# Kernel optimization log

Measured on AMD Instinct MI355X. Metric: run time of the kernel, lower is better.

## Reference

```python
import jax, jax.numpy as jnp
import numpy as np

D = 1024
H = 16
T = D // H  # head dim; attention() scales by sqrt(Q.size(2)) == sqrt(T)
B = 4
S = 2048


def setup_inputs() -> dict:
    key = jax.random.key(0)
    ks = jax.random.split(key, 11)
    lim = 1.0 / np.sqrt(D)  # nn.Linear default init range
    inp = {
        "Q": jax.random.normal(ks[0], (B, S, D), jnp.float32),
        "K": jax.random.normal(ks[1], (B, S, D), jnp.float32),
        "V": jax.random.normal(ks[2], (B, S, D), jnp.float32),
        # per-head Q/K/V projections, stacked: weight [h, t, d], bias [h, t]
        "Wq": jax.random.uniform(ks[3], (H, T, D), jnp.float32, -lim, lim),
        "bq": jax.random.uniform(ks[4], (H, T), jnp.float32, -lim, lim),
        "Wk": jax.random.uniform(ks[5], (H, T, D), jnp.float32, -lim, lim),
        "bk": jax.random.uniform(ks[6], (H, T), jnp.float32, -lim, lim),
        "Wv": jax.random.uniform(ks[7], (H, T, D), jnp.float32, -lim, lim),
        "bv": jax.random.uniform(ks[8], (H, T), jnp.float32, -lim, lim),
        # output projection d -> d
        "Wo": jax.random.uniform(ks[9], (D, D), jnp.float32, -lim, lim),
        "bo": jax.random.uniform(ks[10], (D,), jnp.float32, -lim, lim),
    }
    return inp


def reference(Q, K, V, Wq, bq, Wk, bk, Wv, bv, Wo, bo):
    # Per-head projections, batched over heads: [b, h, s, t]
    q = jnp.einsum("bsd,htd->bhst", Q, Wq) + bq[None, :, None, :]
    k = jnp.einsum("bsd,htd->bhst", K, Wk) + bk[None, :, None, :]
    v = jnp.einsum("bsd,htd->bhst", V, Wv) + bv[None, :, None, :]
    # scaled dot-product attention; scale uses head dim T (Q.size(2) in source)
    scores = jnp.einsum("bhqt,bhkt->bhqk", q, k) / jnp.sqrt(jnp.asarray(T, q.dtype))
    probs = jax.nn.softmax(scores, axis=-1)
    ctx = jnp.einsum("bhqk,bhkt->bhqt", probs, v)
    # concat heads along feature dim (head i -> slice [i*t:(i+1)*t])
    z = ctx.transpose(0, 2, 1, 3).reshape(B, S, D)
    return jnp.einsum("bsd,ed->bse", z, Wo) + bo
```

## Files before the change

### kernel.cpp

```cpp
#include <hip/hip_runtime.h>

typedef unsigned short u16;
typedef unsigned int u32;
typedef __bf16 bf16x8 __attribute__((ext_vector_type(8)));
typedef __bf16 bf16x2 __attribute__((ext_vector_type(2)));
typedef float f32x4 __attribute__((ext_vector_type(4)));
typedef float f32x16 __attribute__((ext_vector_type(16)));
typedef unsigned int u32x2v __attribute__((ext_vector_type(2)));

#define BB 4
#define SS 2048
#define DD 1024
#define HH 16
#define TT 64

#define QSCALE 0.18033688011112042f

__device__ __forceinline__ u16 f32_to_bf16(float f) {
    unsigned int u = __float_as_uint(f);
    u += 0x7fffu + ((u >> 16) & 1u);
    return (u16)(u >> 16);
}

__device__ __forceinline__ u32 pack_bf16x2(float a, float b) {
    bf16x2 t;
    t[0] = (__bf16)a;
    t[1] = (__bf16)b;
    return __builtin_bit_cast(u32, t);
}

__device__ __forceinline__ void pswap(u32& x, u32& y) {
#if __has_builtin(__builtin_amdgcn_permlane32_swap)
    u32x2v r = __builtin_amdgcn_permlane32_swap(x, y, false, false);
    x = r[0];
    y = r[1];
#else
    u32 sx = __shfl_xor(y, 32);
    u32 sy = __shfl_xor(x, 32);
    bool lo = (threadIdx.x & 32) == 0;
    u32 nx = lo ? x : sx;
    u32 ny = lo ? sy : y;
    x = nx;
    y = ny;
#endif
}

#define GLDS(g, l) __builtin_amdgcn_global_load_lds(                              \
    (const __attribute__((address_space(1))) void*)(g),                            \
    (__attribute__((address_space(3))) void*)(l), 16, 0, 0)

struct PackArgs {
    const float* s[4];
    u16* d[4];
};

__global__ __launch_bounds__(256) void pack_multi(PackArgs a) {
    const float* __restrict__ src = a.s[blockIdx.y];
    u16* __restrict__ dst = a.d[blockIdx.y];
    int i = (blockIdx.x * 256 + threadIdx.x) * 8;
    float4 x = *(const float4*)(src + i);
    float4 y = *(const float4*)(src + i + 4);
    ushort4 o0, o1;
    o0.x = f32_to_bf16(x.x); o0.y = f32_to_bf16(x.y);
    o0.z = f32_to_bf16(x.z); o0.w = f32_to_bf16(x.w);
    o1.x = f32_to_bf16(y.x); o1.y = f32_to_bf16(y.y);
    o1.z = f32_to_bf16(y.z); o1.w = f32_to_bf16(y.w);
    *(ushort4*)(dst + i)     = o0;
    *(ushort4*)(dst + i + 4) = o1;
}

#define GEMM_CORE(Aptr, Wptr)                                                      \
    __shared__ u16 lds_a[128 * 64];                                                \
    __shared__ u16 lds_b[128 * 64];                                                \
    const int tid = threadIdx.x;                                                   \
    const int w = tid >> 6, l = tid & 63;                                          \
    const int bm = blockIdx.y * 128;                                               \
    const int bn = blockIdx.x * 128;                                               \
    const int wm = (w >> 1) * 64;                                                  \
    const int wn = (w & 1) * 64;                                                   \
    const int srow = l >> 3;                                                       \
    const int scol = (l & 7) * 16;                                                 \
    f32x4 acc[4][4] = {};                                                          \
    const char* Abase = (const char*)(Aptr) + (size_t)bm * 2048;                   \
    const char* Bbase = (const char*)(Wptr) + (size_t)bn * 2048;                   \
    for (int kt = 0; kt < 1024; kt += 64) {                                        \
        _Pragma("unroll")                                                          \
        for (int j = 0; j < 4; ++j) {                                              \
            int chunk = w * 4 + j;                                                 \
            int r = chunk * 8 + srow;                                              \
            int csrc = scol ^ ((r & 7) << 4);                                      \
            GLDS(Abase + (size_t)r * 2048 + kt * 2 + csrc, &lds_a[chunk * 512]);   \
            GLDS(Bbase + (size_t)r * 2048 + kt * 2 + csrc, &lds_b[chunk * 512]);   \
        }                                                                          \
        __syncthreads();                                                           \
        _Pragma("unroll")                                                          \
        for (int ks = 0; ks < 2; ++ks) {                                           \
            bf16x8 af[4], bfr[4];                                                  \
            _Pragma("unroll")                                                      \
            for (int i = 0; i < 4; ++i) {                                          \
                int ra = wm + i * 16 + (l & 15);                                   \
                int ba = (ks * 64 + ((l >> 4) << 4)) ^ ((ra & 7) << 4);            \
                af[i] = *(const bf16x8*)((const char*)lds_a + ra * 128 + ba);      \
                int rb = wn + i * 16 + (l & 15);                                   \
                int bb2 = (ks * 64 + ((l >> 4) << 4)) ^ ((rb & 7) << 4);           \
                bfr[i] = *(const bf16x8*)((const char*)lds_b + rb * 128 + bb2);    \
            }                                                                      \
            _Pragma("unroll")                                                      \
            for (int mi = 0; mi < 4; ++mi)                                         \
                _Pragma("unroll")                                                  \
                for (int ni = 0; ni < 4; ++ni)                                     \
                    acc[mi][ni] = __builtin_amdgcn_mfma_f32_16x16x32_bf16(         \
                        af[mi], bfr[ni], acc[mi][ni], 0, 0, 0);                    \
        }                                                                          \
        __syncthreads();                                                           \
    }

struct QkvArgs {
    const u16* A[3];
    const u16* W[3];
    const float* bias[3];
    u16* out[3];
};

__global__ __launch_bounds__(256, 2) void gemm_qkv(QkvArgs args) {
    const int mode = blockIdx.z;
    const u16* A = args.A[mode];
    const u16* Wp = args.W[mode];
    const float* bias = args.bias[mode];
    u16* Cb = args.out[mode];

    GEMM_CORE(A, Wp)

    const int mq = (l >> 4) << 2;
    const float scale = (mode == 0) ? QSCALE : 1.0f;
#pragma unroll
    for (int mi = 0; mi < 4; ++mi) {
#pragma unroll
        for (int ni = 0; ni < 4; ++ni) {
            int m0 = bm + wm + mi * 16 + mq;
            int n  = bn + wn + ni * 16 + (l & 15);
            float bv = bias[n];
            f32x4 v = acc[mi][ni];
            if (mode == 2) {
                int bi = m0 >> 11, s0 = m0 & 2047;
                int hi = n >> 6, t = n & 63;
                size_t base = ((size_t)((bi * 16 + hi) * 64 + t)) * 2048 + s0;
                ushort4 pk;
                pk.x = f32_to_bf16(v[0] + bv);
                pk.y = f32_to_bf16(v[1] + bv);
                pk.z = f32_to_bf16(v[2] + bv);
                pk.w = f32_to_bf16(v[3] + bv);
                *(ushort4*)(&Cb[base]) = pk;
            } else {
#pragma unroll
                for (int r = 0; r < 4; ++r) {
                    int m = m0 + r;
                    size_t addr = ((size_t)(((m >> 11) * 16 + (n >> 6)) * 2048 + (m & 2047))) * 64
                                  + (n & 63);
                    Cb[addr] = f32_to_bf16((v[r] + bv) * scale);
                }
            }
        }
    }
}

__global__ __launch_bounds__(256, 2) void gemm_out(
    const u16* __restrict__ A, const u16* __restrict__ Wp,
    const float* __restrict__ bias, float* __restrict__ Cf)
{
    GEMM_CORE(A, Wp)

    const int mq = (l >> 4) << 2;
#pragma unroll
    for (int mi = 0; mi < 4; ++mi) {
#pragma unroll
        for (int ni = 0; ni < 4; ++ni) {
            int m0 = bm + wm + mi * 16 + mq;
            int n  = bn + wn + ni * 16 + (l & 15);
            float bv = bias[n];
            f32x4 v = acc[mi][ni];
#pragma unroll
            for (int r = 0; r < 4; ++r)
                Cf[(size_t)(m0 + r) * 1024 + n] = v[r] + bv;
        }
    }
}

union PbU {
    u32 d[4];
    bf16x8 v;
};

__global__ __launch_bounds__(256, 4) void attn_kernel(
    const u16* __restrict__ qh,
    const u16* __restrict__ kh,
    const u16* __restrict__ vt,
    u16* __restrict__ z)
{
    __shared__ u16 k_lds[2][64 * 64];
    __shared__ u16 v_lds[2][64 * 64];
    const int tid = threadIdx.x;
    const int w = tid >> 6, l = tid & 63;
    const int l31 = l & 31, h2 = l >> 5;
    const int bh = blockIdx.x;
    const int qb = blockIdx.y * 128;
    const size_t hbase = (size_t)bh * (2048 * 64);

    const int qrow = qb + w * 32 + l31;
    bf16x8 qf[4];
    {
        const char* qp = (const char*)(qh + hbase) + (size_t)qrow * 128 + (h2 << 4);
#pragma unroll
        for (int ks = 0; ks < 4; ++ks)
            qf[ks] = *(const bf16x8*)(qp + ks * 32);
    }

    f32x16 ctx0 = {}, ctx1 = {};
    float lsum = 0.f;

    const int grow = (w >> 1) * 32 + l31;
    const int cch  = 4 * (w & 1) + h2;
    const char* kp = (const char*)(kh + hbase) + (size_t)grow * 128 + cch * 16;
    const char* vp = (const char*)(vt + hbase) + (size_t)grow * 4096 + cch * 16;
    const int dofs = (w >> 1) * 2048 + (w & 1) * 1024;
    u16* kdst[2] = { &k_lds[0][dofs], &k_lds[1][dofs] };
    u16* vdst[2] = { &v_lds[0][dofs], &v_lds[1][dofs] };

#define ASTAGE(NB)                                                                 \
    do {                                                                           \
        GLDS(kp, kdst[NB]);          GLDS(kp + 32, kdst[NB] + 512);                \
        GLDS(vp, vdst[NB]);          GLDS(vp + 32, vdst[NB] + 512);                \
        kp += 8192; vp += 128;                                                     \
    } while (0)

    ASTAGE(0);
    __syncthreads();

#define ABODY(CB, NB, PF)                                                          \
    {                                                                              \
        if (PF) ASTAGE(NB);                                                        \
        f32x16 sfr0 = {}, sfr1 = {};                                               \
        __builtin_amdgcn_s_setprio(1);                                             \
        _Pragma("unroll")                                                          \
        for (int ks = 0; ks < 4; ++ks) {                                           \
            int co = (ks << 10) + (h2 << 9) + (l31 << 4);    \
            const char* kb0 = (const char*)k_lds[CB] + co;                         \
            bf16x8 kf0 = *(const bf16x8*)(kb0);                                    \
            bf16x8 kf1 = *(const bf16x8*)(kb0 + 4096);                             \
            sfr0 = __builtin_amdgcn_mfma_f32_32x32x16_bf16(kf0, qf[ks], sfr0, 0, 0, 0); \
            sfr1 = __builtin_amdgcn_mfma_f32_32x32x16_bf16(kf1, qf[ks], sfr1, 0, 0, 0); \
        }                                                                          \
        __builtin_amdgcn_s_setprio(0);                                             \
            \
        uint2 Qd0[4], Qd1[4];                                                      \
        float psum = 0.f;                                                          \
        _Pragma("unroll")                                                          \
        for (int m = 0; m < 4; ++m) {                                              \
            float a0 = __builtin_amdgcn_exp2f(sfr0[4 * m + 0]);                    \
            float a1 = __builtin_amdgcn_exp2f(sfr0[4 * m + 1]);                    \
            float a2 = __builtin_amdgcn_exp2f(sfr0[4 * m + 2]);                    \
            float a3 = __builtin_amdgcn_exp2f(sfr0[4 * m + 3]);                    \
            float b0 = __builtin_amdgcn_exp2f(sfr1[4 * m + 0]);                    \
            float b1 = __builtin_amdgcn_exp2f(sfr1[4 * m + 1]);                    \
            float b2 = __builtin_amdgcn_exp2f(sfr1[4 * m + 2]);                    \
            float b3 = __builtin_amdgcn_exp2f(sfr1[4 * m + 3]);                    \
            psum += ((a0 + a1) + (a2 + a3)) + ((b0 + b1) + (b2 + b3));             \
            Qd0[m] = make_uint2(pack_bf16x2(a0, a1), pack_bf16x2(a2, a3));         \
            Qd1[m] = make_uint2(pack_bf16x2(b0, b1), pack_bf16x2(b2, b3));         \
        }                                                                          \
        lsum += psum;                                                              \
                         \
        __builtin_amdgcn_s_setprio(1);                                             \
        _Pragma("unroll")                                                          \
        for (int ks = 0; ks < 4; ++ks) {                                           \
            u32 x0, x1, y0, y1;                                                    \
            if (ks == 0) { x0 = Qd0[0].x; x1 = Qd0[0].y; y0 = Qd0[1].x; y1 = Qd0[1].y; } \
            else if (ks == 1) { x0 = Qd0[2].x; x1 = Qd0[2].y; y0 = Qd0[3].x; y1 = Qd0[3].y; } \
            else if (ks == 2) { x0 = Qd1[0].x; x1 = Qd1[0].y; y0 = Qd1[1].x; y1 = Qd1[1].y; } \
            else { x0 = Qd1[2].x; x1 = Qd1[2].y; y0 = Qd1[3].x; y1 = Qd1[3].y; }   \
            pswap(x0, y0);                                                         \
            pswap(x1, y1);                                                         \
            PbU pu;                                                                \
            pu.d[0] = x0; pu.d[1] = x1; pu.d[2] = y0; pu.d[3] = y1;                \
            int co = (ks << 10) + (h2 << 9) + (l31 << 4);                          \
            const char* vb0 = (const char*)v_lds[CB] + co;                         \
            bf16x8 vf0 = *(const bf16x8*)(vb0);                                    \
            bf16x8 vf1 = *(const bf16x8*)(vb0 + 4096);                             \
            ctx0 = __builtin_amdgcn_mfma_f32_32x32x16_bf16(vf0, pu.v, ctx0, 0, 0, 0); \
            ctx1 = __builtin_amdgcn_mfma_f32_32x32x16_bf16(vf1, pu.v, ctx1, 0, 0, 0); \
        }                                                                          \
        __builtin_amdgcn_s_setprio(0);                                             \
        __syncthreads();                                                           \
    }

    for (int tt = 0; tt < 32; tt += 2) {
        ABODY(0, 1, true)
        ABODY(1, 0, (tt < 30))
    }
#undef ABODY
#undef ASTAGE

    float rsum = lsum + __shfl_xor(lsum, 32);
    float rinv = 1.0f / rsum;

    const int b = bh >> 4, hd = bh & 15;
    u16* zrow = z + ((size_t)(b * 2048 + qrow)) * 1024 + hd * 64 + (h2 << 2);
#pragma unroll
    for (int m = 0; m < 4; ++m) {
        ushort4 o0, o1;
        o0.x = f32_to_bf16(ctx0[4 * m + 0] * rinv);
        o0.y = f32_to_bf16(ctx0[4 * m + 1] * rinv);
        o0.z = f32_to_bf16(ctx0[4 * m + 2] * rinv);
        o0.w = f32_to_bf16(ctx0[4 * m + 3] * rinv);
        o1.x = f32_to_bf16(ctx1[4 * m + 0] * rinv);
        o1.y = f32_to_bf16(ctx1[4 * m + 1] * rinv);
        o1.z = f32_to_bf16(ctx1[4 * m + 2] * rinv);
        o1.w = f32_to_bf16(ctx1[4 * m + 3] * rinv);
        *(ushort4*)(zrow + 8 * m)      = o0;
        *(ushort4*)(zrow + 8 * m + 32) = o1;
    }
}

extern "C" void kernel_launch(void* const* d_in, const int* in_sizes, int n_in,
                              void* d_out, int out_size, void* d_ws, size_t ws_size,
                              hipStream_t stream) {
    const float* Q  = (const float*)d_in[0];
    const float* K  = (const float*)d_in[1];
    const float* V  = (const float*)d_in[2];
    const float* Wq = (const float*)d_in[3];
    const float* bq = (const float*)d_in[4];
    const float* Wk = (const float*)d_in[5];
    const float* bk = (const float*)d_in[6];
    const float* Wv = (const float*)d_in[7];
    const float* bv = (const float*)d_in[8];
    const float* Wo = (const float*)d_in[9];
    const float* bo = (const float*)d_in[10];

    const int ACT = BB * SS * DD;
    const int WEL = DD * DD;

    u16* ws  = (u16*)d_ws;
    u16* Qb  = ws;
    u16* Kb  = Qb + ACT;
    u16* Vb  = Kb + ACT;
    u16* Wqb = Vb + ACT;
    u16* Wkb = Wqb + WEL;
    u16* Wvb = Wkb + WEL;
    u16* Wob = Wvb + WEL;
    u16* qhb = Wob + WEL;
    u16* khb = qhb + ACT;
    u16* vtb = khb + ACT;
    u16* zb  = vtb + ACT;

    PackArgs pa;
    pa.s[0] = Q;  pa.s[1] = K;  pa.s[2] = V;  pa.s[3] = nullptr;
    pa.d[0] = Qb; pa.d[1] = Kb; pa.d[2] = Vb; pa.d[3] = nullptr;
    pack_multi<<<dim3(ACT / 2048, 3), 256, 0, stream>>>(pa);

    PackArgs pb;
    pb.s[0] = Wq;  pb.s[1] = Wk;  pb.s[2] = Wv;  pb.s[3] = Wo;
    pb.d[0] = Wqb; pb.d[1] = Wkb; pb.d[2] = Wvb; pb.d[3] = Wob;
    pack_multi<<<dim3(WEL / 2048, 4), 256, 0, stream>>>(pb);

    QkvArgs qa;
    qa.A[0] = Qb;  qa.A[1] = Kb;  qa.A[2] = Vb;
    qa.W[0] = Wqb; qa.W[1] = Wkb; qa.W[2] = Wvb;
    qa.bias[0] = bq; qa.bias[1] = bk; qa.bias[2] = bv;
    qa.out[0] = qhb; qa.out[1] = khb; qa.out[2] = vtb;
    gemm_qkv<<<dim3(8, 64, 3), 256, 0, stream>>>(qa);

    attn_kernel<<<dim3(64, 16), 256, 0, stream>>>(qhb, khb, vtb, zb);

    gemm_out<<<dim3(8, 64), 256, 0, stream>>>(zb, Wob, bo, (float*)d_out);
}
```

Baseline: 206.4 us.

## Store Q/K/V projections in pre-tiled layout matching attention LDS fragments

The projection GEMM epilogue now writes Q, K and V^T into a blocked layout of 64-row tiles, split into 32-wide sub-blocks of 8-element chunks, matching the order the attention kernel reads them. The attention kernel then loads each K/V tile as contiguous 1 KB chunks per wave and reads Q fragments with simple strides. This is meant to make the global-to-LDS loads fully contiguous and coalesced instead of strided row gathers. The risk is that the GEMM epilogue scatter becomes less coalesced, and any mismatch in index math would corrupt results.

```diff
diff --git a/kernel.cpp b/kernel.cpp
--- a/kernel.cpp
+++ b/kernel.cpp
@@ -141,23 +141,25 @@
             int n  = bn + wn + ni * 16 + (l & 15);
             float bv = bias[n];
             f32x4 v = acc[mi][ni];
+            int hh = n >> 6, t = n & 63;
             if (mode == 2) {
-                int bi = m0 >> 11, s0 = m0 & 2047;
-                int hi = n >> 6, t = n & 63;
-                size_t base = ((size_t)((bi * 16 + hi) * 64 + t)) * 2048 + s0;
-                ushort4 pk;
-                pk.x = f32_to_bf16(v[0] + bv);
-                pk.y = f32_to_bf16(v[1] + bv);
-                pk.z = f32_to_bf16(v[2] + bv);
-                pk.w = f32_to_bf16(v[3] + bv);
-                *(ushort4*)(&Cb[base]) = pk;
+                int b = m0 >> 11, s2 = m0 & 2047;
+                size_t idx = (size_t)(b * 16 + hh) * 131072
+                           + (s2 >> 6) * 4096 + (t >> 5) * 2048
+                           + ((s2 & 63) >> 3) * 256 + (t & 31) * 8 + (s2 & 7);
+                uint2 pk2;
+                pk2.x = pack_bf16x2(v[0] + bv, v[1] + bv);
+                pk2.y = pack_bf16x2(v[2] + bv, v[3] + bv);
+                *(uint2*)(&Cb[idx]) = pk2;
             } else {
 #pragma unroll
                 for (int r = 0; r < 4; ++r) {
                     int m = m0 + r;
-                    size_t addr = ((size_t)(((m >> 11) * 16 + (n >> 6)) * 2048 + (m & 2047))) * 64
-                                  + (n & 63);
-                    Cb[addr] = f32_to_bf16((v[r] + bv) * scale);
+                    int b = m >> 11, s2 = m & 2047;
+                    size_t idx = (size_t)(b * 16 + hh) * 131072
+                               + (s2 >> 6) * 4096 + ((s2 >> 5) & 1) * 2048
+                               + (t >> 3) * 256 + (s2 & 31) * 8 + (t & 7);
+                    Cb[idx] = f32_to_bf16((v[r] + bv) * scale);
                 }
             }
         }
@@ -204,33 +206,33 @@
     const int l31 = l & 31, h2 = l >> 5;
     const int bh = blockIdx.x;
     const int qb = blockIdx.y * 128;
-    const size_t hbase = (size_t)bh * (2048 * 64);
+    const size_t hb2 = (size_t)bh * 262144;
 
     const int qrow = qb + w * 32 + l31;
     bf16x8 qf[4];
     {
-        const char* qp = (const char*)(qh + hbase) + (size_t)qrow * 128 + (h2 << 4);
+        const char* qp = (const char*)qh + hb2
+                       + (size_t)(blockIdx.y * 2 + (w >> 1)) * 8192
+                       + (w & 1) * 4096 + (h2 << 9) + (l31 << 4);
 #pragma unroll
         for (int ks = 0; ks < 4; ++ks)
-            qf[ks] = *(const bf16x8*)(qp + ks * 32);
+            qf[ks] = *(const bf16x8*)(qp + ks * 1024);
     }
 
     f32x16 ctx0 = {}, ctx1 = {};
     float lsum = 0.f;
 
-    const int grow = (w >> 1) * 32 + l31;
-    const int cch  = 4 * (w & 1) + h2;
-    const char* kp = (const char*)(kh + hbase) + (size_t)grow * 128 + cch * 16;
-    const char* vp = (const char*)(vt + hbase) + (size_t)grow * 4096 + cch * 16;
-    const int dofs = (w >> 1) * 2048 + (w & 1) * 1024;
+    const int dofs = w * 1024;
+    const char* kp = (const char*)kh + hb2 + dofs * 2 + (l << 4);
+    const char* vp = (const char*)vt + hb2 + dofs * 2 + (l << 4);
     u16* kdst[2] = { &k_lds[0][dofs], &k_lds[1][dofs] };
     u16* vdst[2] = { &v_lds[0][dofs], &v_lds[1][dofs] };
 
 #define ASTAGE(NB)                                                                 \
     do {                                                                           \
-        GLDS(kp, kdst[NB]);          GLDS(kp + 32, kdst[NB] + 512);                \
-        GLDS(vp, vdst[NB]);          GLDS(vp + 32, vdst[NB] + 512);                \
-        kp += 8192; vp += 128;                                                     \
+        GLDS(kp, kdst[NB]);          GLDS(kp + 1024, kdst[NB] + 512);              \
+        GLDS(vp, vdst[NB]);          GLDS(vp + 1024, vdst[NB] + 512);              \
+        kp += 8192; vp += 8192;                                                    \
     } while (0)
 
     ASTAGE(0);
```

Result: faster. 199.2 us (-3.5%).
